# Kernel optimization log

Measured on AMD Instinct MI355X. Metric: run time of the kernel, lower is better.

The kernel has to match this reference:

```python
import jax, jax.numpy as jnp
import numpy as np

B, N, E, HID, ED, NH = 2, 10000, 160000, 128, 32, 8
HD = HID // NH  # head_dim = 16
EPS = 1e-5


def setup_inputs() -> dict:
    key = jax.random.key(0)
    ks = jax.random.split(key, 12)
    s = 0.05  # keep pre-tanh activations in a sane range
    return {
        "h": jax.random.normal(ks[0], (B, N, HID), jnp.float32),
        "edge_attr": jax.random.normal(ks[1], (B, E, ED), jnp.float32),
        "edge_index": jax.random.randint(ks[2], (E, 2), 0, N),
        "Wq": jax.random.normal(ks[3], (HID, HID), jnp.float32) * s,
        "bq": jnp.zeros((HID,), jnp.float32),
        "Wk": jax.random.normal(ks[4], (HID, HID), jnp.float32) * s,
        "bk": jnp.zeros((HID,), jnp.float32),
        "Wv": jax.random.normal(ks[5], (HID, HID), jnp.float32) * s,
        "bv": jnp.zeros((HID,), jnp.float32),
        "We": jax.random.normal(ks[6], (HID, ED), jnp.float32) * s,
        "be": jnp.zeros((HID,), jnp.float32),
        "attn_vec": jax.random.normal(ks[7], (NH, HD), jnp.float32) * 0.02,
        "Ws": jax.random.normal(ks[8], (HID, HID), jnp.float32) * s,
        "bs": jnp.zeros((HID,), jnp.float32),
        "Wa": jax.random.normal(ks[9], (HID, HID), jnp.float32) * s,
        "ba": jnp.zeros((HID,), jnp.float32),
        "ln_g": jnp.ones((HID,), jnp.float32),
        "ln_b": jnp.zeros((HID,), jnp.float32),
    }


def reference(h, edge_attr, edge_index, Wq, bq, Wk, bk, Wv, bv, We, be,
              attn_vec, Ws, bs, Wa, ba, ln_g, ln_b):
    src = edge_index[:, 0]
    dst = edge_index[:, 1]
    b, n, hid = h.shape
    e_cnt = src.shape[0]

    h_src = h[:, src, :]  # [B,E,HID]
    h_dst = h[:, dst, :]

    q = (h_dst @ Wq.T + bq).reshape(b, e_cnt, NH, HD)
    k = (h_src @ Wk.T + bk).reshape(b, e_cnt, NH, HD)
    v = (h_src @ Wv.T + bv).reshape(b, e_cnt, NH, HD)
    e = (edge_attr @ We.T + be).reshape(b, e_cnt, NH, HD)

    # GATv2-style scores: [B,E,NH]
    logits = jnp.einsum('behd,hd->beh', jnp.tanh(q + k + e), attn_vec)
    logits = logits / np.float32(np.sqrt(HD))

    # segment softmax over edges grouped by dst node (stable)
    lt = jnp.transpose(logits, (1, 0, 2))  # [E,B,NH]
    mx = jax.ops.segment_max(lt, dst, num_segments=n)  # [N,B,NH]
    ex = jnp.exp(lt - mx[dst])
    den = jax.ops.segment_sum(ex, dst, num_segments=n)
    alpha = jnp.transpose(ex / den[dst], (1, 0, 2))  # [B,E,NH]

    msg = (alpha[..., None] * (v + e)).reshape(b, e_cnt, hid)  # [B,E,HID]
    agg = jax.ops.segment_sum(jnp.transpose(msg, (1, 0, 2)), dst, num_segments=n)
    agg = jnp.transpose(agg, (1, 0, 2))  # [B,N,HID]

    update = (h @ Ws.T + bs) + (agg @ Wa.T + ba)
    x = h + jax.nn.gelu(update, approximate=False)  # dropout is identity in eval

    mu = jnp.mean(x, axis=-1, keepdims=True)
    var = jnp.var(x, axis=-1, keepdims=True)
    return (x - mu) / jnp.sqrt(var + EPS) * ln_g + ln_b
```

## Files before the change

kernel.cpp:

```cpp
#include <hip/hip_runtime.h>
#include <math.h>
#include <stdint.h>

#define B_   2
#define N_   10000
#define E_   160000
#define HID_ 128
#define ED_  32
#define NH_  8
#define HD_  16
#define ROWS_ (B_ * N_)

using half2_t = __attribute__((ext_vector_type(2))) _Float16;
using f16x8   = __attribute__((ext_vector_type(8))) _Float16;
using f32x4   = __attribute__((ext_vector_type(4))) float;

__device__ __forceinline__ half2_t f2h2(float a, float b) {
    return __builtin_bit_cast(half2_t, __builtin_amdgcn_cvt_pkrtz(a, b));
}
__device__ __forceinline__ uint32_t pkh2(float a, float b) {
    return __builtin_bit_cast(uint32_t, __builtin_amdgcn_cvt_pkrtz(a, b));
}


__global__ void zero_kernel(int* __restrict__ deg, int* __restrict__ cursor, int n) {
    int i = blockIdx.x * 256 + threadIdx.x;
    if (i < n) { deg[i] = 0; cursor[i] = 0; }
}

__global__ void hist_kernel(const int* __restrict__ ei, int* __restrict__ deg, int E) {
    int e = blockIdx.x * 256 + threadIdx.x;
    if (e < E) atomicAdd(&deg[ei[2 * e + 1]], 1);
}

__global__ __launch_bounds__(256) void scan_kernel(const int* __restrict__ deg,
                                                   int* __restrict__ off, int N) {
    __shared__ int sums[256];
    int t = threadIdx.x;
    int chunk = (N + 255) / 256;
    int s0 = t * chunk, s1 = min(N, s0 + chunk);
    int s = 0;
    for (int i = s0; i < s1; ++i) s += deg[i];
    sums[t] = s;
    __syncthreads();
    if (t == 0) {
        int run = 0;
        for (int i = 0; i < 256; ++i) { int v = sums[i]; sums[i] = run; run += v; }
        off[N] = run;
    }
    __syncthreads();
    int run = sums[t];
    for (int i = s0; i < s1; ++i) { off[i] = run; run += deg[i]; }
}

__global__ void fill_kernel(const int* __restrict__ ei, const int* __restrict__ off,
                            int* __restrict__ cursor, int* __restrict__ csr, int E) {
    int e = blockIdx.x * 256 + threadIdx.x;
    if (e < E) {
        int d = ei[2 * e + 1];
        int p = atomicAdd(&cursor[d], 1);
        csr[off[d] + p] = e;
    }
}


#define GM 64
#define LDA 68

__global__ __launch_bounds__(256) void qkvs_kernel(
    const float* __restrict__ h,
    const float* __restrict__ Wq, const float* __restrict__ bq,
    const float* __restrict__ Wk, const float* __restrict__ bk,
    const float* __restrict__ Wv, const float* __restrict__ bv,
    const float* __restrict__ Ws, const float* __restrict__ bs,
    const float* __restrict__ ba,
    float* __restrict__ Q, float* __restrict__ KV, float* __restrict__ S)
{
    __shared__ uint32_t As[GM * LDA];
    __shared__ uint32_t Bs[128 * LDA];
    __shared__ float bsm[128];

    int tid = threadIdx.x;
    int lane = tid & 63;
    int wave = tid >> 6;
    int row0 = blockIdx.x * GM;
    int J0 = blockIdx.y * 128;

    if (tid < 128) {
        int J = J0 + tid;
        float v;
        if (J < 128)      v = bq[J];
        else if (J < 256) v = bk[J - 128];
        else if (J < 384) v = bv[J - 256];
        else              v = bs[J - 384] + ba[J - 384];
        bsm[tid] = v;
    }

    for (int f = tid; f < GM * 32; f += 256) {
        int r = f >> 5, c4 = f & 31;
        long row = row0 + r;
        float4 hv = (row < ROWS_) ? *(const float4*)(h + row * HID_ + c4 * 4)
                                  : make_float4(0.f, 0.f, 0.f, 0.f);
        As[r * LDA + c4 * 2]     = pkh2(hv.x, hv.y);
        As[r * LDA + c4 * 2 + 1] = pkh2(hv.z, hv.w);
    }
    for (int f = tid; f < 128 * 32; f += 256) {
        int jr = f >> 5, c4 = f & 31;
        int J = J0 + jr;
        const float* Wp;
        if (J < 128)      Wp = Wq + (long)J * HID_;
        else if (J < 256) Wp = Wk + (long)(J - 128) * HID_;
        else if (J < 384) Wp = Wv + (long)(J - 256) * HID_;
        else              Wp = Ws + (long)(J - 384) * HID_;
        float4 wv = *(const float4*)(Wp + c4 * 4);
        Bs[jr * LDA + c4 * 2]     = pkh2(wv.x, wv.y);
        Bs[jr * LDA + c4 * 2 + 1] = pkh2(wv.z, wv.w);
    }
    __syncthreads();

    f32x4 acc[8];
    #pragma unroll
    for (int nt = 0; nt < 8; ++nt) {
        float c = bsm[nt * 16 + (lane & 15)];
        acc[nt] = (f32x4){ c, c, c, c };
    }

    int ar = wave * 16 + (lane & 15);
    #pragma unroll
    for (int ks = 0; ks < 4; ++ks) {
        f16x8 a = *(const f16x8*)(As + ar * LDA + ks * 16 + (lane >> 4) * 4);
        #pragma unroll
        for (int nt = 0; nt < 8; ++nt) {
            f16x8 b = *(const f16x8*)(Bs + (nt * 16 + (lane & 15)) * LDA + ks * 16 + (lane >> 4) * 4);
            acc[nt] = __builtin_amdgcn_mfma_f32_16x16x32_f16(a, b, acc[nt], 0, 0, 0);
        }
    }

    #pragma unroll
    for (int nt = 0; nt < 8; ++nt) {
        int J = J0 + nt * 16 + (lane & 15);
        long rbase = row0 + wave * 16 + (lane >> 4) * 4;
        #pragma unroll
        for (int r = 0; r < 4; ++r) {
            long row = rbase + r;
            if (row < ROWS_) {
                float v = acc[nt][r];
                if (J < 128)      Q[row * 128 + J] = v;
                else if (J < 256) KV[row * 256 + 2 * (J - 128)] = v;
                else if (J < 384) KV[row * 256 + 2 * (J - 256) + 1] = v;
                else              S[row * 128 + (J - 384)] = v;
            }
        }
    }
}

__global__ __launch_bounds__(256) void wa_kernel(
    const float* __restrict__ X, const float* __restrict__ Wa, float* __restrict__ A)
{
    __shared__ uint32_t As[GM * LDA];
    __shared__ uint32_t Bs[128 * LDA];

    int tid = threadIdx.x;
    int lane = tid & 63;
    int wave = tid >> 6;
    int row0 = blockIdx.x * GM;

    for (int f = tid; f < GM * 32; f += 256) {
        int r = f >> 5, c4 = f & 31;
        long row = row0 + r;
        float4 hv = (row < ROWS_) ? *(const float4*)(X + row * HID_ + c4 * 4)
                                  : make_float4(0.f, 0.f, 0.f, 0.f);
        As[r * LDA + c4 * 2]     = pkh2(hv.x, hv.y);
        As[r * LDA + c4 * 2 + 1] = pkh2(hv.z, hv.w);
    }
    for (int f = tid; f < 128 * 32; f += 256) {
        int jr = f >> 5, c4 = f & 31;
        float4 wv = *(const float4*)(Wa + (long)jr * HID_ + c4 * 4);
        Bs[jr * LDA + c4 * 2]     = pkh2(wv.x, wv.y);
        Bs[jr * LDA + c4 * 2 + 1] = pkh2(wv.z, wv.w);
    }
    __syncthreads();

    f32x4 acc[8];
    #pragma unroll
    for (int nt = 0; nt < 8; ++nt) acc[nt] = (f32x4){ 0.f, 0.f, 0.f, 0.f };

    int ar = wave * 16 + (lane & 15);
    #pragma unroll
    for (int ks = 0; ks < 4; ++ks) {
        f16x8 a = *(const f16x8*)(As + ar * LDA + ks * 16 + (lane >> 4) * 4);
        #pragma unroll
        for (int nt = 0; nt < 8; ++nt) {
            f16x8 b = *(const f16x8*)(Bs + (nt * 16 + (lane & 15)) * LDA + ks * 16 + (lane >> 4) * 4);
            acc[nt] = __builtin_amdgcn_mfma_f32_16x16x32_f16(a, b, acc[nt], 0, 0, 0);
        }
    }

    #pragma unroll
    for (int nt = 0; nt < 8; ++nt) {
        int J = nt * 16 + (lane & 15);
        long rbase = row0 + wave * 16 + (lane >> 4) * 4;
        #pragma unroll
        for (int r = 0; r < 4; ++r) {
            long row = rbase + r;
            if (row < ROWS_) A[row * 128 + J] = acc[nt][r];
        }
    }
}


template <int CTRL>
__device__ __forceinline__ float dpp_add(float x) {
    int y = __builtin_amdgcn_mov_dpp(__float_as_int(x), CTRL, 0xF, 0xF, true);
    return x + __int_as_float(y);
}
__device__ __forceinline__ float hsum16(float p) {
    p = dpp_add<0xB1>(p);
    p = dpp_add<0x4E>(p);
    p = dpp_add<0x141>(p);
    p = dpp_add<0x140>(p);
    return p;
}


#define NPB 4
#define CHUNK 96
#define EAS 20

__global__ __launch_bounds__(128) void node_kernel(
    const float* __restrict__ edge_attr, const int* __restrict__ ei,
    const float* __restrict__ Q, const float* __restrict__ KV,
    const float* __restrict__ We, const float* __restrict__ be,
    const float* __restrict__ attn_vec,
    const int* __restrict__ off, const int* __restrict__ csr,
    float* __restrict__ agg)
{
    int n0 = blockIdx.x * NPB;
    int b  = blockIdx.y;
    int j  = threadIdx.x;
    long bN = (long)b * N_;

    __shared__ int sL[CHUNK];
    __shared__ uint32_t eaL[CHUNK * EAS];

    half2_t we16[16];
    {
        const float4* We4 = (const float4*)(We + (long)j * ED_);
        #pragma unroll
        for (int c = 0; c < 8; ++c) {
            float4 w = We4[c];
            we16[2 * c]     = f2h2(w.x, w.y);
            we16[2 * c + 1] = f2h2(w.z, w.w);
        }
    }
    float bej = be[j];
    float avj = attn_vec[j];

    float q0 = Q[(bN + n0 + 0) * 128 + j];
    float q1 = Q[(bN + n0 + 1) * 128 + j];
    float q2 = Q[(bN + n0 + 2) * 128 + j];
    float q3 = Q[(bN + n0 + 3) * 128 + j];

    int o0 = off[n0];
    int c1 = off[n0 + 1] - o0, c2 = off[n0 + 2] - o0,
        c3 = off[n0 + 3] - o0, c4_ = off[n0 + 4] - o0;
    int total = c4_;

    const float* eab = edge_attr + (long)b * E_ * ED_;
    const float* KVb = KV + bN * 256;

    float acc0 = 0.f, den0 = 0.f, acc1 = 0.f, den1 = 0.f;
    float acc2 = 0.f, den2 = 0.f, acc3 = 0.f, den3 = 0.f;

    auto edge_body = [&](int i, float qg, float& accg, float& deng) {
        int s = sL[i];
        float2 kv = *(const float2*)(KVb + (long)s * 256 + 2 * j);
        float ej = bej;
        const half2_t* ea = (const half2_t*)(eaL + i * EAS);
        #pragma unroll
        for (int c = 0; c < 16; ++c)
            ej = __builtin_amdgcn_fdot2(we16[c], ea[c], ej, false);
        float y = qg + kv.x + ej;
        float t = 1.f - 2.f * __builtin_amdgcn_rcpf(__expf(2.f * y) + 1.f);
        float p = hsum16(t * avj);
        float ex = __expf(p * 0.25f);
        deng += ex;
        accg += ex * (kv.y + ej);
    };

    auto range_loop = [&](int lo, int hi, float qg, float& accg, float& deng) {
        int i = lo;
        for (; i + 3 < hi; i += 4) {
            edge_body(i, qg, accg, deng);
            edge_body(i + 1, qg, accg, deng);
            edge_body(i + 2, qg, accg, deng);
            edge_body(i + 3, qg, accg, deng);
        }
        for (; i < hi; ++i) edge_body(i, qg, accg, deng);
    };

    for (int tau = 0; tau < total; tau += CHUNK) {
        int rows = min(total - tau, CHUNK);
        __syncthreads();
        for (int t = j; t < rows; t += 128) {
            int e = csr[o0 + tau + t];
            sL[t] = ei[2 * e];
        }
        for (int idx = j; idx < rows * 8; idx += 128) {
            int r = idx >> 3, c = idx & 7;
            int e = csr[o0 + tau + r];
            float4 f = *(const float4*)(eab + (long)e * ED_ + c * 4);
            eaL[r * EAS + 2 * c]     = pkh2(f.x, f.y);
            eaL[r * EAS + 2 * c + 1] = pkh2(f.z, f.w);
        }
        __syncthreads();

        range_loop(max(0 - tau, 0),   min(c1 - tau, rows), q0, acc0, den0);
        range_loop(max(c1 - tau, 0),  min(c2 - tau, rows), q1, acc1, den1);
        range_loop(max(c2 - tau, 0),  min(c3 - tau, rows), q2, acc2, den2);
        range_loop(max(c3 - tau, 0),  min(c4_ - tau, rows), q3, acc3, den3);
    }

    agg[(bN + n0 + 0) * 128 + j] = (c1 > 0)   ? acc0 * __builtin_amdgcn_rcpf(den0) : 0.f;
    agg[(bN + n0 + 1) * 128 + j] = (c2 > c1)  ? acc1 * __builtin_amdgcn_rcpf(den1) : 0.f;
    agg[(bN + n0 + 2) * 128 + j] = (c3 > c2)  ? acc2 * __builtin_amdgcn_rcpf(den2) : 0.f;
    agg[(bN + n0 + 3) * 128 + j] = (c4_ > c3) ? acc3 * __builtin_amdgcn_rcpf(den3) : 0.f;
}


__global__ __launch_bounds__(128) void final_kernel(
    const float* __restrict__ h, const float* __restrict__ S, const float* __restrict__ A,
    const float* __restrict__ ln_g, const float* __restrict__ ln_b,
    float* __restrict__ out)
{
    long row = blockIdx.x;
    int j = threadIdx.x;
    __shared__ float red[4];

    float upd = S[row * 128 + j] + A[row * 128 + j];
    float ge = 0.5f * upd * (1.f + erff(upd * 0.70710678118654752f));
    float x = h[row * 128 + j] + ge;

    float s = x, s2 = x * x;
    #pragma unroll
    for (int m = 1; m < 64; m <<= 1) { s += __shfl_xor(s, m); s2 += __shfl_xor(s2, m); }
    int wv = j >> 6;
    if ((j & 63) == 0) { red[wv] = s; red[2 + wv] = s2; }
    __syncthreads();
    float Sm = red[0] + red[1], S2m = red[2] + red[3];
    float mu = Sm * (1.f / 128.f);
    float var = S2m * (1.f / 128.f) - mu * mu;
    out[row * 128 + j] = (x - mu) * rsqrtf(var + 1e-5f) * ln_g[j] + ln_b[j];
}


extern "C" void kernel_launch(void* const* d_in, const int* in_sizes, int n_in,
                              void* d_out, int out_size, void* d_ws, size_t ws_size,
                              hipStream_t stream) {
    const float* h         = (const float*)d_in[0];
    const float* edge_attr = (const float*)d_in[1];
    const int*   ei        = (const int*)  d_in[2];
    const float* Wq = (const float*)d_in[3];
    const float* bq = (const float*)d_in[4];
    const float* Wk = (const float*)d_in[5];
    const float* bk = (const float*)d_in[6];
    const float* Wv = (const float*)d_in[7];
    const float* bv = (const float*)d_in[8];
    const float* We = (const float*)d_in[9];
    const float* be = (const float*)d_in[10];
    const float* attn_vec = (const float*)d_in[11];
    const float* Ws = (const float*)d_in[12];
    const float* bs = (const float*)d_in[13];
    const float* Wa = (const float*)d_in[14];
    const float* ba = (const float*)d_in[15];
    const float* ln_g = (const float*)d_in[16];
    const float* ln_b = (const float*)d_in[17];
    float* out = (float*)d_out;

    size_t p = 0;
    auto alloc = [&](size_t bytes) { size_t r = p; p += (bytes + 255) & ~(size_t)255; return r; };
    char* ws = (char*)d_ws;
    float* Q    = (float*)(ws + alloc((size_t)ROWS_ * 128 * 4));
    float* KV   = (float*)(ws + alloc((size_t)ROWS_ * 256 * 4));
    float* S    = (float*)(ws + alloc((size_t)ROWS_ * 128 * 4));
    float* agg  = (float*)(ws + alloc((size_t)ROWS_ * 128 * 4));
    int* deg    = (int*)(ws + alloc((size_t)N_ * 4));
    int* cursor = (int*)(ws + alloc((size_t)N_ * 4));
    int* off    = (int*)(ws + alloc((size_t)(N_ + 1) * 4));
    int* csr    = (int*)(ws + alloc((size_t)E_ * 4));
    float* A = Q;
    (void)ws_size;

    zero_kernel<<<(N_ + 255) / 256, 256, 0, stream>>>(deg, cursor, N_);
    hist_kernel<<<(E_ + 255) / 256, 256, 0, stream>>>(ei, deg, E_);
    scan_kernel<<<1, 256, 0, stream>>>(deg, off, N_);
    fill_kernel<<<(E_ + 255) / 256, 256, 0, stream>>>(ei, off, cursor, csr, E_);

    dim3 ggrid((ROWS_ + GM - 1) / GM, 4);
    qkvs_kernel<<<ggrid, 256, 0, stream>>>(h, Wq, bq, Wk, bk, Wv, bv, Ws, bs, ba,
                                           Q, KV, S);

    dim3 grid(N_ / NPB, B_);
    node_kernel<<<grid, 128, 0, stream>>>(edge_attr, ei, Q, KV, We, be, attn_vec,
                                          off, csr, agg);

    dim3 wgrid((ROWS_ + GM - 1) / GM, 1);
    wa_kernel<<<wgrid, 256, 0, stream>>>(agg, Wa, A);

    final_kernel<<<ROWS_, 128, 0, stream>>>(h, S, A, ln_g, ln_b, out);
}
```

Measured before the change: 176.6 us.

## Parallelize scan, halve nodes per block, split edge-dot dependency chain

Replaces the serial single-thread prefix over 256 partial sums with a Hillis-Steele parallel scan in shared memory. The node kernel now handles 2 destination nodes per block instead of 4, with a smaller edge chunk, which doubles the grid size for more parallelism and lower per-block imbalance. The 16-step fdot2 chain for the edge embedding is split into two independent accumulators to expose ILP, and the 1/sqrt(HD) scale is folded into attn_vec. Smaller blocks repeat the per-block We load and conversion more often.

Measured after the change: 177.5 us. No clear change (+0.5%).

```diff
diff --git a/kernel.cpp b/kernel.cpp
--- a/kernel.cpp
+++ b/kernel.cpp
@@ -43,13 +43,15 @@
     for (int i = s0; i < s1; ++i) s += deg[i];
     sums[t] = s;
     __syncthreads();
-    if (t == 0) {
-        int run = 0;
-        for (int i = 0; i < 256; ++i) { int v = sums[i]; sums[i] = run; run += v; }
-        off[N] = run;
-    }
-    __syncthreads();
-    int run = sums[t];
+    #pragma unroll
+    for (int d = 1; d < 256; d <<= 1) {
+        int v = (t >= d) ? sums[t - d] : 0;
+        __syncthreads();
+        sums[t] += v;
+        __syncthreads();
+    }
+    if (t == 255) off[N] = sums[255];
+    int run = sums[t] - s;
     for (int i = s0; i < s1; ++i) { off[i] = run; run += deg[i]; }
 }
 
@@ -223,8 +225,8 @@
 }
 
 
-#define NPB 4
-#define CHUNK 96
+#define NPB 2
+#define CHUNK 64
 #define EAS 20
 
 __global__ __launch_bounds__(128) void node_kernel(
@@ -254,36 +256,35 @@
         }
     }
     float bej = be[j];
-    float avj = attn_vec[j];
+    float avj = attn_vec[j] * 0.25f;
 
     float q0 = Q[(bN + n0 + 0) * 128 + j];
     float q1 = Q[(bN + n0 + 1) * 128 + j];
-    float q2 = Q[(bN + n0 + 2) * 128 + j];
-    float q3 = Q[(bN + n0 + 3) * 128 + j];
 
     int o0 = off[n0];
-    int c1 = off[n0 + 1] - o0, c2 = off[n0 + 2] - o0,
-        c3 = off[n0 + 3] - o0, c4_ = off[n0 + 4] - o0;
-    int total = c4_;
+    int c1 = off[n0 + 1] - o0, c2 = off[n0 + 2] - o0;
+    int total = c2;
 
     const float* eab = edge_attr + (long)b * E_ * ED_;
     const float* KVb = KV + bN * 256;
 
     float acc0 = 0.f, den0 = 0.f, acc1 = 0.f, den1 = 0.f;
-    float acc2 = 0.f, den2 = 0.f, acc3 = 0.f, den3 = 0.f;
 
     auto edge_body = [&](int i, float qg, float& accg, float& deng) {
         int s = sL[i];
         float2 kv = *(const float2*)(KVb + (long)s * 256 + 2 * j);
-        float ej = bej;
         const half2_t* ea = (const half2_t*)(eaL + i * EAS);
-        #pragma unroll
-        for (int c = 0; c < 16; ++c)
-            ej = __builtin_amdgcn_fdot2(we16[c], ea[c], ej, false);
+        float eja = bej, ejb = 0.f;
+        #pragma unroll
+        for (int c = 0; c < 8; ++c) {
+            eja = __builtin_amdgcn_fdot2(we16[c], ea[c], eja, false);
+            ejb = __builtin_amdgcn_fdot2(we16[c + 8], ea[c + 8], ejb, false);
+        }
+        float ej = eja + ejb;
         float y = qg + kv.x + ej;
         float t = 1.f - 2.f * __builtin_amdgcn_rcpf(__expf(2.f * y) + 1.f);
         float p = hsum16(t * avj);
-        float ex = __expf(p * 0.25f);
+        float ex = __expf(p);
         deng += ex;
         accg += ex * (kv.y + ej);
     };
@@ -315,16 +316,12 @@
         }
         __syncthreads();
 
-        range_loop(max(0 - tau, 0),   min(c1 - tau, rows), q0, acc0, den0);
-        range_loop(max(c1 - tau, 0),  min(c2 - tau, rows), q1, acc1, den1);
-        range_loop(max(c2 - tau, 0),  min(c3 - tau, rows), q2, acc2, den2);
-        range_loop(max(c3 - tau, 0),  min(c4_ - tau, rows), q3, acc3, den3);
-    }
-
-    agg[(bN + n0 + 0) * 128 + j] = (c1 > 0)   ? acc0 * __builtin_amdgcn_rcpf(den0) : 0.f;
-    agg[(bN + n0 + 1) * 128 + j] = (c2 > c1)  ? acc1 * __builtin_amdgcn_rcpf(den1) : 0.f;
-    agg[(bN + n0 + 2) * 128 + j] = (c3 > c2)  ? acc2 * __builtin_amdgcn_rcpf(den2) : 0.f;
-    agg[(bN + n0 + 3) * 128 + j] = (c4_ > c3) ? acc3 * __builtin_amdgcn_rcpf(den3) : 0.f;
+        range_loop(max(0 - tau, 0),  min(c1 - tau, rows), q0, acc0, den0);
+        range_loop(max(c1 - tau, 0), min(c2 - tau, rows), q1, acc1, den1);
+    }
+
+    agg[(bN + n0 + 0) * 128 + j] = (c1 > 0)  ? acc0 * __builtin_amdgcn_rcpf(den0) : 0.f;
+    agg[(bN + n0 + 1) * 128 + j] = (c2 > c1) ? acc1 * __builtin_amdgcn_rcpf(den1) : 0.f;
 }
 
 
```

## Fuse Wa GEMM with GELU/LayerNorm epilogue and precompute CSR source indices

Applied to the files above, without the earlier changes.

Merges the Wa projection GEMM and the GELU+residual+LayerNorm final kernel into one kernel whose MFMA epilogue does the row reduction with DPP adds, so the A intermediate is never written and read back. The CSR fill now also stores source node ids, removing a dependent gather through edge_index in the node kernel. It also replaces the zeroing kernel with a memset, switches the serial scan to a Hillis-Steele parallel scan, folds the 1/sqrt(HD) scale into attn_vec, and splits the edge-feature dot product into two accumulator chains. The fused epilogue does strided scalar loads of S and h per lane, which may coalesce less well than the old row-per-block kernel.

Measured after the change: 177.4 us. About the same (+0.4%).

```diff
diff --git a/kernel.cpp b/kernel.cpp
--- a/kernel.cpp
+++ b/kernel.cpp
@@ -22,11 +22,6 @@
     return __builtin_bit_cast(uint32_t, __builtin_amdgcn_cvt_pkrtz(a, b));
 }
 
-
-__global__ void zero_kernel(int* __restrict__ deg, int* __restrict__ cursor, int n) {
-    int i = blockIdx.x * 256 + threadIdx.x;
-    if (i < n) { deg[i] = 0; cursor[i] = 0; }
-}
 
 __global__ void hist_kernel(const int* __restrict__ ei, int* __restrict__ deg, int E) {
     int e = blockIdx.x * 256 + threadIdx.x;
@@ -43,23 +38,28 @@
     for (int i = s0; i < s1; ++i) s += deg[i];
     sums[t] = s;
     __syncthreads();
-    if (t == 0) {
-        int run = 0;
-        for (int i = 0; i < 256; ++i) { int v = sums[i]; sums[i] = run; run += v; }
-        off[N] = run;
-    }
-    __syncthreads();
-    int run = sums[t];
+    #pragma unroll
+    for (int d = 1; d < 256; d <<= 1) {
+        int v = (t >= d) ? sums[t - d] : 0;
+        __syncthreads();
+        sums[t] += v;
+        __syncthreads();
+    }
+    if (t == 255) off[N] = sums[255];
+    int run = sums[t] - s;
     for (int i = s0; i < s1; ++i) { off[i] = run; run += deg[i]; }
 }
 
 __global__ void fill_kernel(const int* __restrict__ ei, const int* __restrict__ off,
-                            int* __restrict__ cursor, int* __restrict__ csr, int E) {
+                            int* __restrict__ cursor, int* __restrict__ csr,
+                            int* __restrict__ srcs, int E) {
     int e = blockIdx.x * 256 + threadIdx.x;
     if (e < E) {
-        int d = ei[2 * e + 1];
-        int p = atomicAdd(&cursor[d], 1);
-        csr[off[d] + p] = e;
+        int2 se = *(const int2*)(ei + 2 * e);
+        int p = atomicAdd(&cursor[se.y], 1);
+        int o = off[se.y] + p;
+        csr[o] = e;
+        srcs[o] = se.x;
     }
 }
 
@@ -154,60 +154,6 @@
     }
 }
 
-__global__ __launch_bounds__(256) void wa_kernel(
-    const float* __restrict__ X, const float* __restrict__ Wa, float* __restrict__ A)
-{
-    __shared__ uint32_t As[GM * LDA];
-    __shared__ uint32_t Bs[128 * LDA];
-
-    int tid = threadIdx.x;
-    int lane = tid & 63;
-    int wave = tid >> 6;
-    int row0 = blockIdx.x * GM;
-
-    for (int f = tid; f < GM * 32; f += 256) {
-        int r = f >> 5, c4 = f & 31;
-        long row = row0 + r;
-        float4 hv = (row < ROWS_) ? *(const float4*)(X + row * HID_ + c4 * 4)
-                                  : make_float4(0.f, 0.f, 0.f, 0.f);
-        As[r * LDA + c4 * 2]     = pkh2(hv.x, hv.y);
-        As[r * LDA + c4 * 2 + 1] = pkh2(hv.z, hv.w);
-    }
-    for (int f = tid; f < 128 * 32; f += 256) {
-        int jr = f >> 5, c4 = f & 31;
-        float4 wv = *(const float4*)(Wa + (long)jr * HID_ + c4 * 4);
-        Bs[jr * LDA + c4 * 2]     = pkh2(wv.x, wv.y);
-        Bs[jr * LDA + c4 * 2 + 1] = pkh2(wv.z, wv.w);
-    }
-    __syncthreads();
-
-    f32x4 acc[8];
-    #pragma unroll
-    for (int nt = 0; nt < 8; ++nt) acc[nt] = (f32x4){ 0.f, 0.f, 0.f, 0.f };
-
-    int ar = wave * 16 + (lane & 15);
-    #pragma unroll
-    for (int ks = 0; ks < 4; ++ks) {
-        f16x8 a = *(const f16x8*)(As + ar * LDA + ks * 16 + (lane >> 4) * 4);
-        #pragma unroll
-        for (int nt = 0; nt < 8; ++nt) {
-            f16x8 b = *(const f16x8*)(Bs + (nt * 16 + (lane & 15)) * LDA + ks * 16 + (lane >> 4) * 4);
-            acc[nt] = __builtin_amdgcn_mfma_f32_16x16x32_f16(a, b, acc[nt], 0, 0, 0);
-        }
-    }
-
-    #pragma unroll
-    for (int nt = 0; nt < 8; ++nt) {
-        int J = nt * 16 + (lane & 15);
-        long rbase = row0 + wave * 16 + (lane >> 4) * 4;
-        #pragma unroll
-        for (int r = 0; r < 4; ++r) {
-            long row = rbase + r;
-            if (row < ROWS_) A[row * 128 + J] = acc[nt][r];
-        }
-    }
-}
-
 
 template <int CTRL>
 __device__ __forceinline__ float dpp_add(float x) {
@@ -228,11 +174,12 @@
 #define EAS 20
 
 __global__ __launch_bounds__(128) void node_kernel(
-    const float* __restrict__ edge_attr, const int* __restrict__ ei,
+    const float* __restrict__ edge_attr,
     const float* __restrict__ Q, const float* __restrict__ KV,
     const float* __restrict__ We, const float* __restrict__ be,
     const float* __restrict__ attn_vec,
     const int* __restrict__ off, const int* __restrict__ csr,
+    const int* __restrict__ srcs,
     float* __restrict__ agg)
 {
     int n0 = blockIdx.x * NPB;
@@ -254,7 +201,7 @@
         }
     }
     float bej = be[j];
-    float avj = attn_vec[j];
+    float avj = attn_vec[j] * 0.25f;
 
     float q0 = Q[(bN + n0 + 0) * 128 + j];
     float q1 = Q[(bN + n0 + 1) * 128 + j];
@@ -275,15 +222,18 @@
     auto edge_body = [&](int i, float qg, float& accg, float& deng) {
         int s = sL[i];
         float2 kv = *(const float2*)(KVb + (long)s * 256 + 2 * j);
-        float ej = bej;
+        float eja = bej, ejb = 0.f;
         const half2_t* ea = (const half2_t*)(eaL + i * EAS);
         #pragma unroll
-        for (int c = 0; c < 16; ++c)
-            ej = __builtin_amdgcn_fdot2(we16[c], ea[c], ej, false);
+        for (int c = 0; c < 8; ++c) {
+            eja = __builtin_amdgcn_fdot2(we16[c], ea[c], eja, false);
+            ejb = __builtin_amdgcn_fdot2(we16[c + 8], ea[c + 8], ejb, false);
+        }
+        float ej = eja + ejb;
         float y = qg + kv.x + ej;
         float t = 1.f - 2.f * __builtin_amdgcn_rcpf(__expf(2.f * y) + 1.f);
         float p = hsum16(t * avj);
-        float ex = __expf(p * 0.25f);
+        float ex = __expf(p);
         deng += ex;
         accg += ex * (kv.y + ej);
     };
@@ -302,10 +252,8 @@
     for (int tau = 0; tau < total; tau += CHUNK) {
         int rows = min(total - tau, CHUNK);
         __syncthreads();
-        for (int t = j; t < rows; t += 128) {
-            int e = csr[o0 + tau + t];
-            sL[t] = ei[2 * e];
-        }
+        for (int t = j; t < rows; t += 128)
+            sL[t] = srcs[o0 + tau + t];
         for (int idx = j; idx < rows * 8; idx += 128) {
             int r = idx >> 3, c = idx & 7;
             int e = csr[o0 + tau + r];
@@ -328,29 +276,87 @@
 }
 
 
-__global__ __launch_bounds__(128) void final_kernel(
-    const float* __restrict__ h, const float* __restrict__ S, const float* __restrict__ A,
+__global__ __launch_bounds__(256) void wa_ln_kernel(
+    const float* __restrict__ X,
+    const float* __restrict__ Wa,
+    const float* __restrict__ S, const float* __restrict__ h,
     const float* __restrict__ ln_g, const float* __restrict__ ln_b,
     float* __restrict__ out)
 {
-    long row = blockIdx.x;
-    int j = threadIdx.x;
-    __shared__ float red[4];
-
-    float upd = S[row * 128 + j] + A[row * 128 + j];
-    float ge = 0.5f * upd * (1.f + erff(upd * 0.70710678118654752f));
-    float x = h[row * 128 + j] + ge;
-
-    float s = x, s2 = x * x;
-    #pragma unroll
-    for (int m = 1; m < 64; m <<= 1) { s += __shfl_xor(s, m); s2 += __shfl_xor(s2, m); }
-    int wv = j >> 6;
-    if ((j & 63) == 0) { red[wv] = s; red[2 + wv] = s2; }
+    __shared__ uint32_t As[GM * LDA];
+    __shared__ uint32_t Bs[128 * LDA];
+
+    int tid = threadIdx.x;
+    int lane = tid & 63;
+    int wave = tid >> 6;
+    int row0 = blockIdx.x * GM;
+
+    for (int f = tid; f < GM * 32; f += 256) {
+        int r = f >> 5, c4 = f & 31;
+        long row = row0 + r;
+        float4 hv = (row < ROWS_) ? *(const float4*)(X + row * HID_ + c4 * 4)
+                                  : make_float4(0.f, 0.f, 0.f, 0.f);
+        As[r * LDA + c4 * 2]     = pkh2(hv.x, hv.y);
+        As[r * LDA + c4 * 2 + 1] = pkh2(hv.z, hv.w);
+    }
+    for (int f = tid; f < 128 * 32; f += 256) {
+        int jr = f >> 5, c4 = f & 31;
+        float4 wv = *(const float4*)(Wa + (long)jr * HID_ + c4 * 4);
+        Bs[jr * LDA + c4 * 2]     = pkh2(wv.x, wv.y);
+        Bs[jr * LDA + c4 * 2 + 1] = pkh2(wv.z, wv.w);
+    }
     __syncthreads();
-    float Sm = red[0] + red[1], S2m = red[2] + red[3];
-    float mu = Sm * (1.f / 128.f);
-    float var = S2m * (1.f / 128.f) - mu * mu;
-    out[row * 128 + j] = (x - mu) * rsqrtf(var + 1e-5f) * ln_g[j] + ln_b[j];
+
+    f32x4 acc[8];
+    #pragma unroll
+    for (int nt = 0; nt < 8; ++nt) acc[nt] = (f32x4){ 0.f, 0.f, 0.f, 0.f };
+
+    int ar = wave * 16 + (lane & 15);
+    #pragma unroll
+    for (int ks = 0; ks < 4; ++ks) {
+        f16x8 a = *(const f16x8*)(As + ar * LDA + ks * 16 + (lane >> 4) * 4);
+        #pragma unroll
+        for (int nt = 0; nt < 8; ++nt) {
+            f16x8 b = *(const f16x8*)(Bs + (nt * 16 + (lane & 15)) * LDA + ks * 16 + (lane >> 4) * 4);
+            acc[nt] = __builtin_amdgcn_mfma_f32_16x16x32_f16(a, b, acc[nt], 0, 0, 0);
+        }
+    }
+
+    int lq = lane & 15;
+    float gJ[8], bJ[8];
+    #pragma unroll
+    for (int nt = 0; nt < 8; ++nt) {
+        int J = nt * 16 + lq;
+        gJ[nt] = ln_g[J];
+        bJ[nt] = ln_b[J];
+    }
+    long rbase = row0 + wave * 16 + (lane >> 4) * 4;
+    #pragma unroll
+    for (int r = 0; r < 4; ++r) {
+        long row = rbase + r;
+        if (row < ROWS_) {
+            float xv[8];
+            float sum = 0.f, sum2 = 0.f;
+            #pragma unroll
+            for (int nt = 0; nt < 8; ++nt) {
+                int J = nt * 16 + lq;
+                float upd = acc[nt][r] + S[row * 128 + J];
+                float ge = 0.5f * upd * (1.f + erff(upd * 0.70710678118654752f));
+                float x = h[row * 128 + J] + ge;
+                xv[nt] = x;
+                sum += x;
+                sum2 += x * x;
+            }
+            sum = hsum16(sum);
+            sum2 = hsum16(sum2);
+            float mu = sum * (1.f / 128.f);
+            float var = sum2 * (1.f / 128.f) - mu * mu;
+            float rs = rsqrtf(var + 1e-5f);
+            #pragma unroll
+            for (int nt = 0; nt < 8; ++nt)
+                out[row * 128 + nt * 16 + lq] = (xv[nt] - mu) * rs * gJ[nt] + bJ[nt];
+        }
+    }
 }
 
 
@@ -384,28 +390,27 @@
     float* KV   = (float*)(ws + alloc((size_t)ROWS_ * 256 * 4));
     float* S    = (float*)(ws + alloc((size_t)ROWS_ * 128 * 4));
     float* agg  = (float*)(ws + alloc((size_t)ROWS_ * 128 * 4));
-    int* deg    = (int*)(ws + alloc((size_t)N_ * 4));
-    int* cursor = (int*)(ws + alloc((size_t)N_ * 4));
+    int* dc     = (int*)(ws + alloc((size_t)2 * N_ * 4));
     int* off    = (int*)(ws + alloc((size_t)(N_ + 1) * 4));
     int* csr    = (int*)(ws + alloc((size_t)E_ * 4));
-    float* A = Q;
+    int* srcs   = (int*)(ws + alloc((size_t)E_ * 4));
+    int* deg = dc;
+    int* cursor = dc + N_;
     (void)ws_size;
 
-    zero_kernel<<<(N_ + 255) / 256, 256, 0, stream>>>(deg, cursor, N_);
+    hipMemsetAsync(dc, 0, (size_t)2 * N_ * 4, stream);
     hist_kernel<<<(E_ + 255) / 256, 256, 0, stream>>>(ei, deg, E_);
     scan_kernel<<<1, 256, 0, stream>>>(deg, off, N_);
-    fill_kernel<<<(E_ + 255) / 256, 256, 0, stream>>>(ei, off, cursor, csr, E_);
+    fill_kernel<<<(E_ + 255) / 256, 256, 0, stream>>>(ei, off, cursor, csr, srcs, E_);
 
     dim3 ggrid((ROWS_ + GM - 1) / GM, 4);
     qkvs_kernel<<<ggrid, 256, 0, stream>>>(h, Wq, bq, Wk, bk, Wv, bv, Ws, bs, ba,
                                            Q, KV, S);
 
     dim3 grid(N_ / NPB, B_);
-    node_kernel<<<grid, 128, 0, stream>>>(edge_attr, ei, Q, KV, We, be, attn_vec,
-                                          off, csr, agg);
-
-    dim3 wgrid((ROWS_ + GM - 1) / GM, 1);
-    wa_kernel<<<wgrid, 256, 0, stream>>>(agg, Wa, A);
-
-    final_kernel<<<ROWS_, 128, 0, stream>>>(h, S, A, ln_g, ln_b, out);
-}
+    node_kernel<<<grid, 128, 0, stream>>>(edge_attr, Q, KV, We, be, attn_vec,
+                                          off, csr, srcs, agg);
+
+    wa_ln_kernel<<<(ROWS_ + GM - 1) / GM, 256, 0, stream>>>(agg, Wa, S, h,
+                                                            ln_g, ln_b, out);
+}
```
